# Kernel tuning notes

Measured on AMD Instinct MI355X. Metric: run time of the kernel, lower is better.

The kernel has to match this reference:

```python
import jax, jax.numpy as jnp
import numpy as np

D = 1024       # d_model
H = 16         # num_heads
DK = D // H    # head dim (64)
DFF = 4096     # SwiGLU hidden dim
THETA = 10000.0
EPS = 1e-5
B, S = 2, 2048


def setup_inputs() -> dict:
    key = jax.random.key(0)
    ks = jax.random.split(key, 9)
    p = lambda k, shape: jax.random.normal(k, shape, dtype=jnp.float32) * 0.02
    return {
        "x": jax.random.normal(ks[0], (B, S, D), dtype=jnp.float32),
        "w_q": p(ks[1], (D, D)),   # Linear stores [out, in]
        "w_k": p(ks[2], (D, D)),
        "w_v": p(ks[3], (D, D)),
        "w_o": p(ks[4], (D, D)),
        "ln1_w": jnp.ones((D,), dtype=jnp.float32),
        "ln2_w": jnp.ones((D,), dtype=jnp.float32),
        "w1": p(ks[5], (DFF, D)),  # gate-in proj: d_model -> dff
        "w2": p(ks[6], (D, DFF)),  # down proj:    dff -> d_model
        "w3": p(ks[7], (DFF, D)),  # up proj:      d_model -> dff
    }


def _rmsnorm(x, w):
    xf = x.astype(jnp.float32)
    inv = jax.lax.rsqrt(jnp.mean(xf * xf, axis=-1, keepdims=True) + EPS)
    return (inv * xf * w).astype(x.dtype)


def _rope(x, pos):
    # x: [..., seq, DK]; pos: [seq]
    inv_freq = THETA ** (-(jnp.arange(0, DK, 2, dtype=jnp.float32) / DK))  # [DK/2]
    ang = pos.astype(jnp.float32)[:, None] * inv_freq                      # [seq, DK/2]
    cos, sin = jnp.cos(ang), jnp.sin(ang)
    xe, xo = x[..., ::2], x[..., 1::2]
    re = cos * xe - sin * xo
    ro = sin * xe + cos * xo
    return jnp.stack((re, ro), axis=-1).reshape(x.shape)  # interleave even/odd


def reference(x, w_q, w_k, w_v, w_o, ln1_w, ln2_w, w1, w2, w3):
    b, s, d = x.shape
    pos = jnp.arange(s)

    # --- attention sublayer ---
    h = _rmsnorm(x, ln1_w)
    def proj(w):  # [b,s,d] x [d,d] -> [b,H,s,DK]
        return jnp.einsum('bsd,ed->bse', h, w).reshape(b, s, H, DK).transpose(0, 2, 1, 3)
    q = _rope(proj(w_q), pos)
    k = _rope(proj(w_k), pos)
    v = proj(w_v)

    scores = jnp.einsum('bhqd,bhkd->bhqk', q, k) / (DK ** 0.5)
    causal = jnp.tril(jnp.ones((s, s), dtype=bool))
    scores = jnp.where(causal, scores, -jnp.inf)
    attn = jax.nn.softmax(scores, axis=-1)
    o = jnp.einsum('bhqk,bhkd->bhqd', attn, v).transpose(0, 2, 1, 3).reshape(b, s, d)
    x = x + jnp.einsum('bsd,ed->bse', o, w_o)

    # --- SwiGLU FFN sublayer ---
    h2 = _rmsnorm(x, ln2_w)
    u = jnp.einsum('bsd,fd->bsf', h2, w1)
    g = jnp.einsum('bsd,fd->bsf', h2, w3)
    ffn = jnp.einsum('bsf,df->bsd', u * jax.nn.sigmoid(u) * g, w2)
    return x + ffn
```

## Files before the change

### kernel.cpp

```cpp
#include <hip/hip_runtime.h>

typedef _Float16 half_t;
typedef _Float16 f16x8 __attribute__((ext_vector_type(8)));
typedef _Float16 f16x4 __attribute__((ext_vector_type(4)));
typedef _Float16 f16x2 __attribute__((ext_vector_type(2)));
typedef float fx4 __attribute__((ext_vector_type(4)));

typedef __attribute__((address_space(1))) const unsigned int as1_cuint;
typedef __attribute__((address_space(3))) unsigned int as3_uint;

__device__ __forceinline__ void gld16(const void* g, void* l) {
    __builtin_amdgcn_global_load_lds((as1_cuint*)g, (as3_uint*)l, 16, 0, 0);
}

template<int MODE>
__global__ __launch_bounds__(256, 2)
void gemm_bt(const half_t* __restrict__ A,
             const half_t* __restrict__ B0, const half_t* __restrict__ B1,
             const half_t* __restrict__ B2,
             half_t* o0, half_t* o1, half_t* o2, half_t* o3,
             int M, int N, int K)
{
    __shared__ half_t sA[128 * 32];
    __shared__ half_t sB[128 * 32];
    const int tid = threadIdx.x;
    const int wid = tid >> 6, lane = tid & 63;
    const int lm = lane & 15, lg = lane >> 4;
    const int wr = wid >> 1, wc = wid & 1;
    const int m0 = blockIdx.x * 128, n0 = blockIdx.y * 128;

    const half_t* Bp = B0;
    half_t* outb = o0;
    if (MODE == 1) {
        if (blockIdx.z == 1) { Bp = B1; outb = o1; }
        else if (blockIdx.z == 2) { Bp = B2; outb = o2; }
    }
    if (MODE == 4) {
        if (blockIdx.z == 1) outb = o1;
        else if (blockIdx.z == 2) outb = o2;
        else if (blockIdx.z == 3) outb = o3;
    }

    int Keff = K, koff = 0;
    if (MODE == 4) { Keff = K / gridDim.z; koff = blockIdx.z * Keff; }

    const int srow = tid >> 2;
    const int scolb = ((tid & 3) ^ ((srow >> 1) & 3)) << 4;
    const char* gA = (const char*)(A + (size_t)(m0 + srow) * K + koff) + scolb;
    const char* gB = (const char*)(Bp + (size_t)(n0 + srow) * K + koff) + scolb;
    const size_t rstep = (size_t)64 * K * sizeof(half_t);
    char* lA = (char*)sA + tid * 16;
    char* lB = (char*)sB + tid * 16;

    const int ksw = (lm >> 1) & 3;

    fx4 acc[4][4] = {};

    for (int kt = 0; kt < Keff; kt += 32) {
        gld16(gA, lA);
        gld16(gA + rstep, lA + 4096);
        gld16(gB, lB);
        gld16(gB + rstep, lB + 4096);
        gA += 64; gB += 64;
        __syncthreads();
        f16x8 aF[4], bF[4];
#pragma unroll
        for (int mi = 0; mi < 4; mi++)
            aF[mi] = *(const f16x8*)(sA + (wr * 64 + mi * 16 + lm) * 32 + (lg ^ ksw) * 8);
#pragma unroll
        for (int ni = 0; ni < 4; ni++)
            bF[ni] = *(const f16x8*)(sB + (wc * 64 + ni * 16 + lm) * 32 + (lg ^ ksw) * 8);
#pragma unroll
        for (int mi = 0; mi < 4; mi++)
#pragma unroll
            for (int ni = 0; ni < 4; ni++)
                acc[mi][ni] = __builtin_amdgcn_mfma_f32_16x16x32_f16(aF[mi], bF[ni], acc[mi][ni], 0, 0, 0);
        __syncthreads();
    }

#pragma unroll
    for (int mi = 0; mi < 4; mi++) {
#pragma unroll
        for (int ni = 0; ni < 4; ni++) {
#pragma unroll
            for (int r = 0; r < 4; r++) {
                int m = m0 + wr * 64 + mi * 16 + lg * 4 + r;
                int n = n0 + wc * 64 + ni * 16 + lm;
                float v = acc[mi][ni][r];
                size_t idx = (size_t)m * N + n;
                if (MODE == 1) {
                    int b = m >> 11, s = m & 2047, hh = n >> 6, dk = n & 63;
                    if (blockIdx.z == 2) {
                        outb[((size_t)(b * 16 + hh) * 64 + dk) * 2048 + s] = (half_t)v;
                    } else {
                        outb[((size_t)(b * 16 + hh) * 2048 + s) * 64 + dk] = (half_t)v;
                    }
                } else {
                    outb[idx] = (half_t)v;
                }
            }
        }
    }
}

__global__ __launch_bounds__(256, 2)
void gemm_dual(const half_t* __restrict__ A,
               const half_t* __restrict__ B1, const half_t* __restrict__ B2,
               half_t* __restrict__ out, int M, int N, int K)
{
    __shared__ half_t sA[128 * 32];
    __shared__ half_t sB1[128 * 32];
    __shared__ half_t sB2[128 * 32];
    const int tid = threadIdx.x;
    const int wid = tid >> 6, lane = tid & 63;
    const int lm = lane & 15, lg = lane >> 4;
    const int wr = wid >> 1, wc = wid & 1;
    const int m0 = blockIdx.x * 128, n0 = blockIdx.y * 128;

    const int srow = tid >> 2;
    const int scolb = ((tid & 3) ^ ((srow >> 1) & 3)) << 4;
    const char* gA = (const char*)(A + (size_t)(m0 + srow) * K) + scolb;
    const char* gB1 = (const char*)(B1 + (size_t)(n0 + srow) * K) + scolb;
    const char* gB2 = (const char*)(B2 + (size_t)(n0 + srow) * K) + scolb;
    const size_t rstep = (size_t)64 * K * sizeof(half_t);
    char* lA = (char*)sA + tid * 16;
    char* lB1 = (char*)sB1 + tid * 16;
    char* lB2 = (char*)sB2 + tid * 16;

    const int ksw = (lm >> 1) & 3;

    fx4 accU[4][4] = {};
    fx4 accG[4][4] = {};

    for (int kt = 0; kt < K; kt += 32) {
        gld16(gA, lA);
        gld16(gA + rstep, lA + 4096);
        gld16(gB1, lB1);
        gld16(gB1 + rstep, lB1 + 4096);
        gld16(gB2, lB2);
        gld16(gB2 + rstep, lB2 + 4096);
        gA += 64; gB1 += 64; gB2 += 64;
        __syncthreads();
        f16x8 aF[4], b1F[4], b2F[4];
#pragma unroll
        for (int mi = 0; mi < 4; mi++)
            aF[mi] = *(const f16x8*)(sA + (wr * 64 + mi * 16 + lm) * 32 + (lg ^ ksw) * 8);
#pragma unroll
        for (int ni = 0; ni < 4; ni++) {
            b1F[ni] = *(const f16x8*)(sB1 + (wc * 64 + ni * 16 + lm) * 32 + (lg ^ ksw) * 8);
            b2F[ni] = *(const f16x8*)(sB2 + (wc * 64 + ni * 16 + lm) * 32 + (lg ^ ksw) * 8);
        }
#pragma unroll
        for (int mi = 0; mi < 4; mi++)
#pragma unroll
            for (int ni = 0; ni < 4; ni++) {
                accU[mi][ni] = __builtin_amdgcn_mfma_f32_16x16x32_f16(aF[mi], b1F[ni], accU[mi][ni], 0, 0, 0);
                accG[mi][ni] = __builtin_amdgcn_mfma_f32_16x16x32_f16(aF[mi], b2F[ni], accG[mi][ni], 0, 0, 0);
            }
        __syncthreads();
    }

#pragma unroll
    for (int mi = 0; mi < 4; mi++) {
#pragma unroll
        for (int ni = 0; ni < 4; ni++) {
#pragma unroll
            for (int r = 0; r < 4; r++) {
                int m = m0 + wr * 64 + mi * 16 + lg * 4 + r;
                int n = n0 + wc * 64 + ni * 16 + lm;
                float u = accU[mi][ni][r];
                float g = accG[mi][ni][r];
                out[(size_t)m * N + n] = (half_t)(u / (1.f + __expf(-u)) * g);
            }
        }
    }
}

__global__ __launch_bounds__(256, 4)
void addnorm_k(const float* __restrict__ x,
               const half_t* __restrict__ p0, const half_t* __restrict__ p1,
               const float* __restrict__ w,
               float* __restrict__ outF, half_t* __restrict__ outH)
{
    int row = blockIdx.x * 4 + (threadIdx.x >> 6);
    int lane = threadIdx.x & 63;
    const float4* xr = (const float4*)(x + (size_t)row * 1024);
    const f16x4* p0r = (const f16x4*)(p0 + (size_t)row * 1024);
    const f16x4* p1r = (const f16x4*)(p1 + (size_t)row * 1024);
    float4 v[4];
    float s = 0.f;
#pragma unroll
    for (int i = 0; i < 4; i++) {
        float4 xv = xr[lane + 64 * i];
        f16x4 a0 = p0r[lane + 64 * i];
        f16x4 a1 = p1r[lane + 64 * i];
        v[i].x = xv.x + (float)a0[0] + (float)a1[0];
        v[i].y = xv.y + (float)a0[1] + (float)a1[1];
        v[i].z = xv.z + (float)a0[2] + (float)a1[2];
        v[i].w = xv.w + (float)a0[3] + (float)a1[3];
        s += v[i].x * v[i].x + v[i].y * v[i].y + v[i].z * v[i].z + v[i].w * v[i].w;
    }
#pragma unroll
    for (int o = 32; o > 0; o >>= 1) s += __shfl_xor(s, o);
    float inv = rsqrtf(s * (1.f / 1024.f) + 1e-5f);
    const float4* w4 = (const float4*)w;
    float4* oF = (float4*)(outF + (size_t)row * 1024);
    f16x4* oH = (f16x4*)(outH + (size_t)row * 1024);
#pragma unroll
    for (int i = 0; i < 4; i++) {
        oF[lane + 64 * i] = v[i];
        float4 wv = w4[lane + 64 * i];
        f16x4 ov = { (half_t)(v[i].x * inv * wv.x), (half_t)(v[i].y * inv * wv.y),
                     (half_t)(v[i].z * inv * wv.z), (half_t)(v[i].w * inv * wv.w) };
        oH[lane + 64 * i] = ov;
    }
}

__global__ __launch_bounds__(256, 8)
void reduce4_k(const half_t* __restrict__ p0, const half_t* __restrict__ p1,
               const half_t* __restrict__ p2, const half_t* __restrict__ p3,
               float* __restrict__ out, int n4)
{
    int i = blockIdx.x * 256 + threadIdx.x;
    if (i >= n4) return;
    float4 b = ((const float4*)out)[i];
    f16x4 a0 = ((const f16x4*)p0)[i];
    f16x4 a1 = ((const f16x4*)p1)[i];
    f16x4 a2 = ((const f16x4*)p2)[i];
    f16x4 a3 = ((const f16x4*)p3)[i];
    float4 o = { b.x + (float)a0[0] + (float)a1[0] + (float)a2[0] + (float)a3[0],
                 b.y + (float)a0[1] + (float)a1[1] + (float)a2[1] + (float)a3[1],
                 b.z + (float)a0[2] + (float)a1[2] + (float)a2[2] + (float)a3[2],
                 b.w + (float)a0[3] + (float)a1[3] + (float)a2[3] + (float)a3[3] };
    ((float4*)out)[i] = o;
}

__global__ __launch_bounds__(256, 4)
void rmsnorm_k(const float* __restrict__ x, const float* __restrict__ w,
               half_t* __restrict__ out)
{
    int row = blockIdx.x * 4 + (threadIdx.x >> 6);
    int lane = threadIdx.x & 63;
    const float4* xr = (const float4*)(x + (size_t)row * 1024);
    float4 v[4];
    float s = 0.f;
#pragma unroll
    for (int i = 0; i < 4; i++) {
        v[i] = xr[lane + 64 * i];
        s += v[i].x * v[i].x + v[i].y * v[i].y + v[i].z * v[i].z + v[i].w * v[i].w;
    }
#pragma unroll
    for (int o = 32; o > 0; o >>= 1) s += __shfl_xor(s, o);
    float inv = rsqrtf(s * (1.f / 1024.f) + 1e-5f);
    const float4* w4 = (const float4*)w;
    f16x4* o4 = (f16x4*)(out + (size_t)row * 1024);
#pragma unroll
    for (int i = 0; i < 4; i++) {
        float4 wv = w4[lane + 64 * i];
        f16x4 ov = { (half_t)(v[i].x * inv * wv.x), (half_t)(v[i].y * inv * wv.y),
                     (half_t)(v[i].z * inv * wv.z), (half_t)(v[i].w * inv * wv.w) };
        o4[lane + 64 * i] = ov;
    }
}

struct CastA { const float* s; half_t* d; int n4; };
struct CastArgs { CastA a[7]; };

__global__ void cast_k(CastArgs ca)
{
    CastA a = ca.a[blockIdx.y];
    int i = blockIdx.x * 256 + threadIdx.x;
    if (i >= a.n4) return;
    float4 v = ((const float4*)a.s)[i];
    ((f16x4*)a.d)[i] = (f16x4){ (half_t)v.x, (half_t)v.y, (half_t)v.z, (half_t)v.w };
}

__global__ void rope_k(half_t* Q, half_t* Kv)
{
    int idx = blockIdx.x * 256 + threadIdx.x;
    half_t* P = blockIdx.y ? Kv : Q;
    float scq = blockIdx.y ? 1.0f : 0.125f;
    int i = idx & 31;
    int s = (idx >> 5) & 2047;
    int bh = idx >> 16;
    float f = __expf((float)i * -0.28782313662f);
    float ang = (float)s * f;
    float c = cosf(ang), sn = sinf(ang);
    f16x2* p = (f16x2*)(P + ((size_t)bh * 2048 + s) * 64 + 2 * i);
    f16x2 xv = *p;
    float xe = (float)xv[0], xo = (float)xv[1];
    *p = (f16x2){ (half_t)((c * xe - sn * xo) * scq), (half_t)((sn * xe + c * xo) * scq) };
}

__global__ __launch_bounds__(256, 2)
void attn_k(const half_t* __restrict__ Q, const half_t* __restrict__ K,
            const half_t* __restrict__ VT, half_t* __restrict__ O)
{
    __shared__ half_t sK[128 * 64];
    __shared__ half_t sVT[64 * 128];
    __shared__ half_t sP[4][16 * 128];
    const int tid = threadIdx.x, wid = tid >> 6, lane = tid & 63;
    const int lm = lane & 15, lg = lane >> 4;
    const int p = blockIdx.x, bh = blockIdx.y;
    const int b = bh >> 4, hh = bh & 15;
    const size_t base = (size_t)bh * (2048 * 64);

    const int krow = tid >> 3;
    const int kcsw = ((tid & 7) ^ (krow & 7)) << 4;
    const int vrow = tid >> 4;
    const int vcsw = ((tid & 15) ^ (vrow & 15)) << 4;
    const char* gK = (const char*)(K + base);
    const char* gV = (const char*)(VT + base);
    char* lK = (char*)sK + tid * 16;
    char* lV = (char*)sVT + tid * 16;
    half_t* sPw = sP[wid];

    f16x8 vone;
#pragma unroll
    for (int j = 0; j < 8; j++) vone[j] = (half_t)1.f;

    for (int ph = 0; ph < 2; ph++) {
        const int qt = ph ? (31 - p) : p;
        const int q0 = qt * 64 + wid * 16;
        const int nT = (qt + 2) >> 1;

        f16x8 bQ[2];
#pragma unroll
        for (int ki = 0; ki < 2; ki++)
            bQ[ki] = *(const f16x8*)(Q + base + (size_t)(q0 + lm) * 64 + ki * 32 + lg * 8);

        fx4 oacc[4] = {};
        fx4 lacc = {};

        for (int t = 0; t < nT; t++) {
            const int kv0 = t * 128;
#pragma unroll
            for (int i = 0; i < 4; i++)
                gld16(gK + (size_t)(kv0 + i * 32 + krow) * 128 + kcsw, lK + i * 4096);
#pragma unroll
            for (int i = 0; i < 4; i++)
                gld16(gV + (size_t)(i * 16 + vrow) * 4096 + (size_t)kv0 * 2 + vcsw, lV + i * 4096);
            __syncthreads();

            fx4 st[8] = {};
#pragma unroll
            for (int ki = 0; ki < 2; ki++) {
#pragma unroll
                for (int mi = 0; mi < 8; mi++) {
                    f16x8 aK = *(const f16x8*)(sK + ((mi * 16 + lm) << 6) +
                                               (((ki * 4 + lg) ^ (lm & 7)) << 3));
                    st[mi] = __builtin_amdgcn_mfma_f32_16x16x32_f16(aK, bQ[ki], st[mi], 0, 0, 0);
                }
            }

            const bool diag = (t == nT - 1);
            const int qg = q0 + lm;
#pragma unroll
            for (int mi = 0; mi < 8; mi++) {
                f16x4 ev;
#pragma unroll
                for (int r = 0; r < 4; r++) {
                    float e = __expf(st[mi][r]);
                    if (diag && (kv0 + mi * 16 + lg * 4 + r > qg)) e = 0.f;
                    ev[r] = (half_t)e;
                }
                *(f16x4*)(sPw + (lm << 7) +
                          ((((mi * 2 + (lg >> 1)) ^ lm) << 3) | ((lg & 1) << 2))) = ev;
            }

#pragma unroll
            for (int k2 = 0; k2 < 4; k2++) {
                f16x8 aP = *(const f16x8*)(sPw + (lm << 7) + (((k2 * 4 + lg) ^ lm) << 3));
#pragma unroll
                for (int ni = 0; ni < 4; ni++) {
                    f16x8 bV = *(const f16x8*)(sVT + ((ni * 16 + lm) << 7) +
                                               (((k2 * 4 + lg) ^ lm) << 3));
                    oacc[ni] = __builtin_amdgcn_mfma_f32_16x16x32_f16(aP, bV, oacc[ni], 0, 0, 0);
                }
                lacc = __builtin_amdgcn_mfma_f32_16x16x32_f16(aP, vone, lacc, 0, 0, 0);
            }
            __syncthreads();
        }

        float inv[4];
#pragma unroll
        for (int r = 0; r < 4; r++) inv[r] = 1.f / lacc[r];
#pragma unroll
        for (int ni = 0; ni < 4; ni++)
#pragma unroll
            for (int r = 0; r < 4; r++) {
                int s = q0 + lg * 4 + r;
                O[((size_t)b * 2048 + s) * 1024 + hh * 64 + ni * 16 + lm] =
                    (half_t)(oacc[ni][r] * inv[r]);
            }
    }
}

extern "C" void kernel_launch(void* const* d_in, const int* in_sizes, int n_in,
                              void* d_out, int out_size, void* d_ws, size_t ws_size,
                              hipStream_t stream)
{
    const float* x   = (const float*)d_in[0];
    const float* wq  = (const float*)d_in[1];
    const float* wk  = (const float*)d_in[2];
    const float* wv  = (const float*)d_in[3];
    const float* wo  = (const float*)d_in[4];
    const float* ln1 = (const float*)d_in[5];
    const float* ln2 = (const float*)d_in[6];
    const float* w1  = (const float*)d_in[7];
    const float* w2  = (const float*)d_in[8];
    const float* w3  = (const float*)d_in[9];

    half_t* W = (half_t*)d_ws;
    const size_t Mi = 1048576;
    half_t* wq16 = W;
    half_t* wk16 = W + Mi;
    half_t* wv16 = W + 2 * Mi;
    half_t* wo16 = W + 3 * Mi;
    half_t* w116 = W + 4 * Mi;
    half_t* w316 = W + 8 * Mi;
    half_t* w216 = W + 12 * Mi;
    half_t* h16  = W + 16 * Mi;
    half_t* q16  = W + 20 * Mi;
    half_t* k16  = W + 24 * Mi;
    half_t* vt16 = W + 28 * Mi;
    half_t* a16  = W + 16 * Mi;
    half_t* h216 = W + 32 * Mi;
    half_t* P0   = W + 20 * Mi;
    half_t* P1   = W + 24 * Mi;
    half_t* D0   = W;
    half_t* D1   = W + 4 * Mi;
    half_t* D2   = W + 8 * Mi;
    half_t* D3   = W + 36 * Mi;

    CastArgs ca;
    ca.a[0] = { wq, wq16, 262144 };
    ca.a[1] = { wk, wk16, 262144 };
    ca.a[2] = { wv, wv16, 262144 };
    ca.a[3] = { wo, wo16, 262144 };
    ca.a[4] = { w1, w116, 1048576 };
    ca.a[5] = { w2, w216, 1048576 };
    ca.a[6] = { w3, w316, 1048576 };

    cast_k<<<dim3(4096, 7), 256, 0, stream>>>(ca);
    rmsnorm_k<<<dim3(1024), 256, 0, stream>>>(x, ln1, h16);
    gemm_bt<1><<<dim3(32, 8, 3), 256, 0, stream>>>(h16, wq16, wk16, wv16,
                                                   q16, k16, vt16, nullptr,
                                                   4096, 1024, 1024);
    rope_k<<<dim3(8192, 2), 256, 0, stream>>>(q16, k16);
    attn_k<<<dim3(16, 32), 256, 0, stream>>>(q16, k16, vt16, h16);
    gemm_bt<4><<<dim3(32, 8, 2), 256, 0, stream>>>(h16, wo16, nullptr, nullptr,
                                                   P0, P1, nullptr, nullptr,
                                                   4096, 1024, 1024);
    addnorm_k<<<dim3(1024), 256, 0, stream>>>(x, P0, P1, ln2,
                                              (float*)d_out, h216);
    gemm_dual<<<dim3(32, 32), 256, 0, stream>>>(h216, w116, w316, a16,
                                                4096, 4096, 1024);
    gemm_bt<4><<<dim3(32, 8, 4), 256, 0, stream>>>(a16, w216, nullptr, nullptr,
                                                   D0, D1, D2, D3,
                                                   4096, 1024, 4096);
    reduce4_k<<<dim3(4096), 256, 0, stream>>>(D0, D1, D2, D3, (float*)d_out, 1048576);
    (void)in_sizes; (void)n_in; (void)out_size; (void)ws_size;
}
```

Baseline: 381.5 us.

## Rewrite SwiGLU dual GEMM with 8-wave 256x128 tiles and double-buffered LDS pipeline

Replaces the gate/up dual GEMM with a 512-thread kernel using 256x128 output tiles and K-steps of 64. LDS is double-buffered and the next tile's global-to-LDS loads are interleaved with MFMA phases, using explicit waitcnt, barriers and setprio. The aim is to hide memory latency and raise per-block data reuse for the largest GEMM. The trade-off is hard-coded K=1024 loop counts and more LDS (96KB per block), which may limit occupancy.

```diff
diff --git a/kernel.cpp b/kernel.cpp
--- a/kernel.cpp
+++ b/kernel.cpp
@@ -103,71 +103,109 @@
     }
 }
 
-__global__ __launch_bounds__(256, 2)
-void gemm_dual(const half_t* __restrict__ A,
-               const half_t* __restrict__ B1, const half_t* __restrict__ B2,
-               half_t* __restrict__ out, int M, int N, int K)
-{
-    __shared__ half_t sA[128 * 32];
-    __shared__ half_t sB1[128 * 32];
-    __shared__ half_t sB2[128 * 32];
+__device__ __forceinline__ const f16x8* fragp(const half_t* s, int row, int cc) {
+    return (const f16x8*)(s + (((row << 3) | (cc ^ (row & 7))) << 3));
+}
+
+#define PH(P, STAGE, WAITV)                                                   \
+  {                                                                           \
+    f16x8 aF[2][2];                                                           \
+    _Pragma("unroll") for (int i = 0; i < 2; i++)                             \
+      _Pragma("unroll") for (int kk = 0; kk < 2; kk++)                        \
+        aF[i][kk] = *fragp(cA, wr * 128 + (2 * (P) + i) * 16 + lm, kk * 4 + lg); \
+    STAGE;                                                                    \
+    __builtin_amdgcn_s_barrier();                                             \
+    asm volatile("s_waitcnt lgkmcnt(0)" ::: "memory");                        \
+    __builtin_amdgcn_sched_barrier(0);                                        \
+    __builtin_amdgcn_s_setprio(1);                                            \
+    _Pragma("unroll") for (int kk = 0; kk < 2; kk++)                          \
+      _Pragma("unroll") for (int i = 0; i < 2; i++)                           \
+        _Pragma("unroll") for (int ni = 0; ni < 2; ni++) {                    \
+          accU[2 * (P) + i][ni] = __builtin_amdgcn_mfma_f32_16x16x32_f16(     \
+              aF[i][kk], b1F[ni][kk], accU[2 * (P) + i][ni], 0, 0, 0);        \
+          accG[2 * (P) + i][ni] = __builtin_amdgcn_mfma_f32_16x16x32_f16(     \
+              aF[i][kk], b2F[ni][kk], accG[2 * (P) + i][ni], 0, 0, 0);        \
+        }                                                                     \
+    __builtin_amdgcn_s_setprio(0);                                            \
+    WAITV;                                                                    \
+    __builtin_amdgcn_s_barrier();                                             \
+  }
+
+#define KTILE(CUR, LAST)                                                      \
+  {                                                                           \
+    const half_t* cA  = sA[CUR];                                              \
+    const half_t* cB1 = sB1[CUR];                                             \
+    const half_t* cB2 = sB2[CUR];                                             \
+    char* nA  = (char*)sA[1 - (CUR)]  + tid * 16;                             \
+    char* nB1 = (char*)sB1[1 - (CUR)] + tid * 16;                             \
+    char* nB2 = (char*)sB2[1 - (CUR)] + tid * 16;                             \
+    f16x8 b1F[2][2], b2F[2][2];                                               \
+    _Pragma("unroll") for (int ni = 0; ni < 2; ni++)                          \
+      _Pragma("unroll") for (int kk = 0; kk < 2; kk++) {                      \
+        b1F[ni][kk] = *fragp(cB1, wc * 32 + ni * 16 + lm, kk * 4 + lg);       \
+        b2F[ni][kk] = *fragp(cB2, wc * 32 + ni * 16 + lm, kk * 4 + lg);       \
+      }                                                                       \
+    PH(0, { if (!(LAST)) { gld16(gB1, nB1); gld16(gB1 + rstep, nB1 + 8192); } }, {}) \
+    PH(1, { if (!(LAST)) { gld16(gB2, nB2); gld16(gB2 + rstep, nB2 + 8192); } },     \
+          { if (LAST) { asm volatile("s_waitcnt vmcnt(0)" ::: "memory"); }    \
+            else      { asm volatile("s_waitcnt vmcnt(4)" ::: "memory"); } }) \
+    PH(2, { if (!(LAST)) { gld16(gA, nA); gld16(gA + 2 * rstep, nA + 2 * 8192); } }, {}) \
+    PH(3, { if (!(LAST)) { gld16(gA + rstep, nA + 8192);                      \
+                           gld16(gA + 3 * rstep, nA + 3 * 8192); } },         \
+          { if (!(LAST)) { asm volatile("s_waitcnt vmcnt(2)" ::: "memory"); } }) \
+    gA += 128; gB1 += 128; gB2 += 128;                                        \
+  }
+
+__global__ __launch_bounds__(512, 2)
+void gemm_dual8(const half_t* __restrict__ A,
+                const half_t* __restrict__ B1, const half_t* __restrict__ B2,
+                half_t* __restrict__ out, int M, int N, int K)
+{
+    __shared__ half_t sA[2][256 * 64];
+    __shared__ half_t sB1[2][128 * 64];
+    __shared__ half_t sB2[2][128 * 64];
     const int tid = threadIdx.x;
     const int wid = tid >> 6, lane = tid & 63;
     const int lm = lane & 15, lg = lane >> 4;
-    const int wr = wid >> 1, wc = wid & 1;
-    const int m0 = blockIdx.x * 128, n0 = blockIdx.y * 128;
-
-    const int srow = tid >> 2;
-    const int scolb = ((tid & 3) ^ ((srow >> 1) & 3)) << 4;
-    const char* gA = (const char*)(A + (size_t)(m0 + srow) * K) + scolb;
-    const char* gB1 = (const char*)(B1 + (size_t)(n0 + srow) * K) + scolb;
-    const char* gB2 = (const char*)(B2 + (size_t)(n0 + srow) * K) + scolb;
+    const int wr = wid >> 2, wc = wid & 3;
+    const int m0 = blockIdx.x * 256, n0 = blockIdx.y * 128;
+
+    const int srow = tid >> 3;
+    const int schunk = (tid & 7) ^ (srow & 7);
+    const char* gA  = (const char*)(A  + (size_t)(m0 + srow) * K) + schunk * 16;
+    const char* gB1 = (const char*)(B1 + (size_t)(n0 + srow) * K) + schunk * 16;
+    const char* gB2 = (const char*)(B2 + (size_t)(n0 + srow) * K) + schunk * 16;
     const size_t rstep = (size_t)64 * K * sizeof(half_t);
-    char* lA = (char*)sA + tid * 16;
-    char* lB1 = (char*)sB1 + tid * 16;
-    char* lB2 = (char*)sB2 + tid * 16;
-
-    const int ksw = (lm >> 1) & 3;
-
-    fx4 accU[4][4] = {};
-    fx4 accG[4][4] = {};
-
-    for (int kt = 0; kt < K; kt += 32) {
-        gld16(gA, lA);
-        gld16(gA + rstep, lA + 4096);
-        gld16(gB1, lB1);
-        gld16(gB1 + rstep, lB1 + 4096);
-        gld16(gB2, lB2);
-        gld16(gB2 + rstep, lB2 + 4096);
-        gA += 64; gB1 += 64; gB2 += 64;
-        __syncthreads();
-        f16x8 aF[4], b1F[4], b2F[4];
-#pragma unroll
-        for (int mi = 0; mi < 4; mi++)
-            aF[mi] = *(const f16x8*)(sA + (wr * 64 + mi * 16 + lm) * 32 + (lg ^ ksw) * 8);
-#pragma unroll
-        for (int ni = 0; ni < 4; ni++) {
-            b1F[ni] = *(const f16x8*)(sB1 + (wc * 64 + ni * 16 + lm) * 32 + (lg ^ ksw) * 8);
-            b2F[ni] = *(const f16x8*)(sB2 + (wc * 64 + ni * 16 + lm) * 32 + (lg ^ ksw) * 8);
-        }
-#pragma unroll
-        for (int mi = 0; mi < 4; mi++)
-#pragma unroll
-            for (int ni = 0; ni < 4; ni++) {
-                accU[mi][ni] = __builtin_amdgcn_mfma_f32_16x16x32_f16(aF[mi], b1F[ni], accU[mi][ni], 0, 0, 0);
-                accG[mi][ni] = __builtin_amdgcn_mfma_f32_16x16x32_f16(aF[mi], b2F[ni], accG[mi][ni], 0, 0, 0);
-            }
-        __syncthreads();
-    }
-
-#pragma unroll
-    for (int mi = 0; mi < 4; mi++) {
-#pragma unroll
-        for (int ni = 0; ni < 4; ni++) {
+
+    {
+        char* dA  = (char*)sA[0]  + tid * 16;
+        char* dB1 = (char*)sB1[0] + tid * 16;
+        char* dB2 = (char*)sB2[0] + tid * 16;
+        gld16(gB1, dB1);            gld16(gB1 + rstep, dB1 + 8192);
+        gld16(gB2, dB2);            gld16(gB2 + rstep, dB2 + 8192);
+        gld16(gA, dA);              gld16(gA + 2 * rstep, dA + 2 * 8192);
+        gld16(gA + rstep, dA + 8192); gld16(gA + 3 * rstep, dA + 3 * 8192);
+        gA += 128; gB1 += 128; gB2 += 128;
+        asm volatile("s_waitcnt vmcnt(2)" ::: "memory");
+        __builtin_amdgcn_s_barrier();
+    }
+
+    fx4 accU[8][2] = {};
+    fx4 accG[8][2] = {};
+
+#pragma unroll 1
+    for (int t = 0; t < 14; t += 2) { KTILE(0, 0) KTILE(1, 0) }
+    KTILE(0, 0)
+    KTILE(1, 1)
+
+#pragma unroll
+    for (int mi = 0; mi < 8; mi++) {
+#pragma unroll
+        for (int ni = 0; ni < 2; ni++) {
 #pragma unroll
             for (int r = 0; r < 4; r++) {
-                int m = m0 + wr * 64 + mi * 16 + lg * 4 + r;
-                int n = n0 + wc * 64 + ni * 16 + lm;
+                int m = m0 + wr * 128 + mi * 16 + lg * 4 + r;
+                int n = n0 + wc * 32 + ni * 16 + lm;
                 float u = accU[mi][ni][r];
                 float g = accG[mi][ni][r];
                 out[(size_t)m * N + n] = (half_t)(u / (1.f + __expf(-u)) * g);
@@ -454,8 +492,8 @@
                                                    4096, 1024, 1024);
     addnorm_k<<<dim3(1024), 256, 0, stream>>>(x, P0, P1, ln2,
                                               (float*)d_out, h216);
-    gemm_dual<<<dim3(32, 32), 256, 0, stream>>>(h216, w116, w316, a16,
-                                                4096, 4096, 1024);
+    gemm_dual8<<<dim3(16, 32), 512, 0, stream>>>(h216, w116, w316, a16,
+                                                 4096, 4096, 1024);
     gemm_bt<4><<<dim3(32, 8, 4), 256, 0, stream>>>(a16, w216, nullptr, nullptr,
                                                    D0, D1, D2, D3,
                                                    4096, 1024, 4096);
```

New measurement: 380.0 us. Within noise of the previous version (-0.4%).

## Rewrite SwiGLU dual GEMM as 256x128 eight-wave pipelined kernel with LDS exchange

Applied to the files above, without the earlier changes.

Replaces the 128x128, 4-wave gate/up GEMM with a 256x128, 8-wave kernel. Half the waves compute the w1 product and half the w3 product, and the results are combined through shared memory in the epilogue. The K loop now uses BK=64 double-buffered direct-to-LDS loads interleaved with four MFMA phases, plus explicit waitcnt, barriers and setprio. The aim is more reuse of the A tile, better overlap of global loads with compute, and fewer accumulator registers per wave. The trade-offs are a 128KB LDS footprint that limits occupancy, extra barriers, and a loop count hard-coded for K=1024.

```diff
diff --git a/kernel.cpp b/kernel.cpp
--- a/kernel.cpp
+++ b/kernel.cpp
@@ -103,76 +103,172 @@
     }
 }
 
-__global__ __launch_bounds__(256, 2)
-void gemm_dual(const half_t* __restrict__ A,
-               const half_t* __restrict__ B1, const half_t* __restrict__ B2,
-               half_t* __restrict__ out, int M, int N, int K)
-{
-    __shared__ half_t sA[128 * 32];
-    __shared__ half_t sB1[128 * 32];
-    __shared__ half_t sB2[128 * 32];
+__global__ __launch_bounds__(512, 2)
+void gemm_dual9(const half_t* __restrict__ A,
+                const half_t* __restrict__ B1, const half_t* __restrict__ B2,
+                half_t* __restrict__ out, int M, int N, int K)
+{
+    __shared__ half_t smem[65536];
     const int tid = threadIdx.x;
     const int wid = tid >> 6, lane = tid & 63;
     const int lm = lane & 15, lg = lane >> 4;
-    const int wr = wid >> 1, wc = wid & 1;
-    const int m0 = blockIdx.x * 128, n0 = blockIdx.y * 128;
-
-    const int srow = tid >> 2;
-    const int scolb = ((tid & 3) ^ ((srow >> 1) & 3)) << 4;
-    const char* gA = (const char*)(A + (size_t)(m0 + srow) * K) + scolb;
-    const char* gB1 = (const char*)(B1 + (size_t)(n0 + srow) * K) + scolb;
-    const char* gB2 = (const char*)(B2 + (size_t)(n0 + srow) * K) + scolb;
-    const size_t rstep = (size_t)64 * K * sizeof(half_t);
-    char* lA = (char*)sA + tid * 16;
-    char* lB1 = (char*)sB1 + tid * 16;
-    char* lB2 = (char*)sB2 + tid * 16;
-
-    const int ksw = (lm >> 1) & 3;
-
-    fx4 accU[4][4] = {};
-    fx4 accG[4][4] = {};
-
-    for (int kt = 0; kt < K; kt += 32) {
-        gld16(gA, lA);
-        gld16(gA + rstep, lA + 4096);
-        gld16(gB1, lB1);
-        gld16(gB1 + rstep, lB1 + 4096);
-        gld16(gB2, lB2);
-        gld16(gB2 + rstep, lB2 + 4096);
-        gA += 64; gB1 += 64; gB2 += 64;
-        __syncthreads();
-        f16x8 aF[4], b1F[4], b2F[4];
-#pragma unroll
-        for (int mi = 0; mi < 4; mi++)
-            aF[mi] = *(const f16x8*)(sA + (wr * 64 + mi * 16 + lm) * 32 + (lg ^ ksw) * 8);
-#pragma unroll
-        for (int ni = 0; ni < 4; ni++) {
-            b1F[ni] = *(const f16x8*)(sB1 + (wc * 64 + ni * 16 + lm) * 32 + (lg ^ ksw) * 8);
-            b2F[ni] = *(const f16x8*)(sB2 + (wc * 64 + ni * 16 + lm) * 32 + (lg ^ ksw) * 8);
-        }
-#pragma unroll
-        for (int mi = 0; mi < 4; mi++)
+    const int wr = wid >> 2, wc = wid & 3;
+    const int m0 = blockIdx.x * 256, n0 = blockIdx.y * 128;
+
+    const size_t KB = (size_t)K * 2;
+    const int srow = tid >> 3;
+    const int schunk = (tid & 7) ^ (srow & 7);
+    const char* pA  = (const char*)A  + (size_t)(m0 + srow) * KB + schunk * 16;
+    const char* pB0 = (const char*)B1 + (size_t)(n0 + srow) * KB + schunk * 16;
+    const char* pB1 = (const char*)B2 + (size_t)(n0 + srow) * KB + schunk * 16;
+    const char* pA00 = pA;
+    const char* pA0h = pA + 64 * KB;
+    const char* pA10 = pA + 128 * KB;
+    const char* pA1h = pA + 192 * KB;
+    const char* pB0h = pB0 + 64 * KB;
+    const char* pB1h = pB1 + 64 * KB;
+
+    char* const lbase = (char*)smem + tid * 16;
+#define LDST(buf, half, sec) (lbase + (buf) * 65536 + (half) * 16384 + (sec) * 8192)
+
+    const int lA = lm * 128;
+    const int swz0 = ((lg ^ (lm & 7)) << 4);
+    const int swz1 = (((4 + lg) ^ (lm & 7)) << 4);
+    const char* aBase = (const char*)smem + wr * 16384 + lA;
+    const char* bBase = (const char*)smem + (2 + (wc >> 1)) * 16384 + (wc & 1) * 8192 + lA;
+
+    gld16(pA00, LDST(0, 0, 0));
+    gld16(pB0,  LDST(0, 2, 0)); gld16(pB0h, LDST(0, 2, 1));
+    gld16(pA0h, LDST(0, 0, 1)); gld16(pA10, LDST(0, 1, 0)); gld16(pA1h, LDST(0, 1, 1));
+    gld16(pB1,  LDST(0, 3, 0)); gld16(pB1h, LDST(0, 3, 1));
+    gld16(pA00 + 128, LDST(1, 0, 0));
+    gld16(pB0 + 128,  LDST(1, 2, 0)); gld16(pB0h + 128, LDST(1, 2, 1));
+    gld16(pA0h + 128, LDST(1, 0, 1)); gld16(pA10 + 128, LDST(1, 1, 0)); gld16(pA1h + 128, LDST(1, 1, 1));
+    asm volatile("s_waitcnt vmcnt(6)" ::: "memory");
+    __builtin_amdgcn_s_barrier();
+
+    fx4 acc[8][4] = {};
+
+#pragma unroll
+    for (int t = 0; t < 16; ++t) {
+        const int BO = (t & 1) * 65536;
+        const int s1 = (t + 1) * 128, s2 = (t + 2) * 128;
+        const int b1 = (t + 1) & 1, b2 = t & 1;
+        f16x8 aLo[4][2], aHi[4][2], bA[2][2], bB[2][2];
+
+#pragma unroll
+        for (int mi = 0; mi < 4; mi++) {
+            aLo[mi][0] = *(const f16x8*)(aBase + BO + mi * 2048 + swz0);
+            aLo[mi][1] = *(const f16x8*)(aBase + BO + mi * 2048 + swz1);
+        }
+#pragma unroll
+        for (int ni = 0; ni < 2; ni++) {
+            bA[ni][0] = *(const f16x8*)(bBase + BO + ni * 2048 + swz0);
+            bA[ni][1] = *(const f16x8*)(bBase + BO + ni * 2048 + swz1);
+        }
+        if (t < 15) { gld16(pB1 + s1, LDST(b1, 3, 0)); gld16(pB1h + s1, LDST(b1, 3, 1)); }
+        asm volatile("s_waitcnt lgkmcnt(8)" ::: "memory");
+        __builtin_amdgcn_s_barrier();
+        asm volatile("s_waitcnt lgkmcnt(0)" ::: "memory");
+        __builtin_amdgcn_sched_barrier(0);
+        __builtin_amdgcn_s_setprio(1);
+#pragma unroll
+        for (int kk = 0; kk < 2; kk++)
+#pragma unroll
+            for (int mi = 0; mi < 4; mi++)
+#pragma unroll
+                for (int ni = 0; ni < 2; ni++)
+                    acc[mi][ni] = __builtin_amdgcn_mfma_f32_16x16x32_f16(aLo[mi][kk], bA[ni][kk], acc[mi][ni], 0, 0, 0);
+        __builtin_amdgcn_s_setprio(0);
+        __builtin_amdgcn_s_barrier();
+
+#pragma unroll
+        for (int ni = 0; ni < 2; ni++) {
+            bB[ni][0] = *(const f16x8*)(bBase + BO + (2 + ni) * 2048 + swz0);
+            bB[ni][1] = *(const f16x8*)(bBase + BO + (2 + ni) * 2048 + swz1);
+        }
+        if (t < 14) { gld16(pA00 + s2, LDST(b2, 0, 0)); }
+        __builtin_amdgcn_s_barrier();
+        asm volatile("s_waitcnt lgkmcnt(0)" ::: "memory");
+        __builtin_amdgcn_sched_barrier(0);
+        __builtin_amdgcn_s_setprio(1);
+#pragma unroll
+        for (int kk = 0; kk < 2; kk++)
+#pragma unroll
+            for (int mi = 0; mi < 4; mi++)
+#pragma unroll
+                for (int ni = 0; ni < 2; ni++)
+                    acc[mi][2 + ni] = __builtin_amdgcn_mfma_f32_16x16x32_f16(aLo[mi][kk], bB[ni][kk], acc[mi][2 + ni], 0, 0, 0);
+        __builtin_amdgcn_s_setprio(0);
+        __builtin_amdgcn_s_barrier();
+
+#pragma unroll
+        for (int mi = 0; mi < 4; mi++) {
+            aHi[mi][0] = *(const f16x8*)(aBase + BO + (4 + mi) * 2048 + swz0);
+            aHi[mi][1] = *(const f16x8*)(aBase + BO + (4 + mi) * 2048 + swz1);
+        }
+        if (t < 14) { gld16(pB0 + s2, LDST(b2, 2, 0)); gld16(pB0h + s2, LDST(b2, 2, 1)); }
+        __builtin_amdgcn_s_barrier();
+        asm volatile("s_waitcnt lgkmcnt(0)" ::: "memory");
+        __builtin_amdgcn_sched_barrier(0);
+        __builtin_amdgcn_s_setprio(1);
+#pragma unroll
+        for (int kk = 0; kk < 2; kk++)
+#pragma unroll
+            for (int mi = 0; mi < 4; mi++)
+#pragma unroll
+                for (int ni = 0; ni < 2; ni++)
+                    acc[4 + mi][2 + ni] = __builtin_amdgcn_mfma_f32_16x16x32_f16(aHi[mi][kk], bB[ni][kk], acc[4 + mi][2 + ni], 0, 0, 0);
+        __builtin_amdgcn_s_setprio(0);
+        __builtin_amdgcn_s_barrier();
+
+        if (t < 14) {
+            gld16(pA0h + s2, LDST(b2, 0, 1));
+            gld16(pA10 + s2, LDST(b2, 1, 0));
+            gld16(pA1h + s2, LDST(b2, 1, 1));
+        }
+        __builtin_amdgcn_s_barrier();
+        __builtin_amdgcn_sched_barrier(0);
+        __builtin_amdgcn_s_setprio(1);
+#pragma unroll
+        for (int kk = 0; kk < 2; kk++)
+#pragma unroll
+            for (int mi = 0; mi < 4; mi++)
+#pragma unroll
+                for (int ni = 0; ni < 2; ni++)
+                    acc[4 + mi][ni] = __builtin_amdgcn_mfma_f32_16x16x32_f16(aHi[mi][kk], bA[ni][kk], acc[4 + mi][ni], 0, 0, 0);
+        __builtin_amdgcn_s_setprio(0);
+        if (t < 14)      { asm volatile("s_waitcnt vmcnt(6)" ::: "memory"); }
+        else if (t == 14){ asm volatile("s_waitcnt vmcnt(0)" ::: "memory"); }
+        __builtin_amdgcn_s_barrier();
+    }
+#undef LDST
+
+    float* gb = (float*)smem;
+    if (wc >= 2) {
+        const int gw = wr * 2 + (wc - 2);
+#pragma unroll
+        for (int mi = 0; mi < 8; mi++)
+#pragma unroll
+            for (int ni = 0; ni < 4; ni++)
+                *(fx4*)((char*)gb + ((((gw * 8 + mi) * 4 + ni) * 64 + lane) << 4)) = acc[mi][ni];
+    }
+    __syncthreads();
+    if (wc < 2) {
+        const int gw = wr * 2 + wc;
+#pragma unroll
+        for (int mi = 0; mi < 8; mi++)
 #pragma unroll
             for (int ni = 0; ni < 4; ni++) {
-                accU[mi][ni] = __builtin_amdgcn_mfma_f32_16x16x32_f16(aF[mi], b1F[ni], accU[mi][ni], 0, 0, 0);
-                accG[mi][ni] = __builtin_amdgcn_mfma_f32_16x16x32_f16(aF[mi], b2F[ni], accG[mi][ni], 0, 0, 0);
+                fx4 gv = *(const fx4*)((const char*)gb + ((((gw * 8 + mi) * 4 + ni) * 64 + lane) << 4));
+#pragma unroll
+                for (int r = 0; r < 4; r++) {
+                    int m = m0 + wr * 128 + mi * 16 + lg * 4 + r;
+                    int n = n0 + wc * 64 + ni * 16 + lm;
+                    float u = acc[mi][ni][r], g = gv[r];
+                    out[(size_t)m * N + n] = (half_t)(u / (1.f + __expf(-u)) * g);
+                }
             }
-        __syncthreads();
-    }
-
-#pragma unroll
-    for (int mi = 0; mi < 4; mi++) {
-#pragma unroll
-        for (int ni = 0; ni < 4; ni++) {
-#pragma unroll
-            for (int r = 0; r < 4; r++) {
-                int m = m0 + wr * 64 + mi * 16 + lg * 4 + r;
-                int n = n0 + wc * 64 + ni * 16 + lm;
-                float u = accU[mi][ni][r];
-                float g = accG[mi][ni][r];
-                out[(size_t)m * N + n] = (half_t)(u / (1.f + __expf(-u)) * g);
-            }
-        }
     }
 }
 
@@ -454,11 +550,11 @@
                                                    4096, 1024, 1024);
     addnorm_k<<<dim3(1024), 256, 0, stream>>>(x, P0, P1, ln2,
                                               (float*)d_out, h216);
-    gemm_dual<<<dim3(32, 32), 256, 0, stream>>>(h216, w116, w316, a16,
-                                                4096, 4096, 1024);
+    gemm_dual9<<<dim3(16, 32), 512, 0, stream>>>(h216, w116, w316, a16,
+                                                 4096, 4096, 1024);
     gemm_bt<4><<<dim3(32, 8, 4), 256, 0, stream>>>(a16, w216, nullptr, nullptr,
                                                    D0, D1, D2, D3,
-                                                   4096, 1024, 4096);
+                                                   1048576 / 256, 1024, 4096);
     reduce4_k<<<dim3(4096), 256, 0, stream>>>(D0, D1, D2, D3, (float*)d_out, 1048576);
     (void)in_sizes; (void)n_in; (void)out_size; (void)ws_size;
 }
```

After: 394.3 us. 1.03x slower.
